# Performance work log

Hardware: AMD Instinct MI355X
Metric: run time of the kernel (lower is better)

The kernel has to match this reference:

```python
import jax, jax.numpy as jnp
import numpy as np

N = 20000
E = 320000
IN_DIM = 128
HID = 64
HEADS = 8
OUT_DIM = 128
NEG_SLOPE = 0.2  # PyG GATConv default leaky_relu slope


def _glorot(key, shape):
    fan_in = shape[0] if len(shape) > 1 else shape[-1]
    return jax.random.normal(key, shape, dtype=jnp.float32) / jnp.sqrt(jnp.float32(fan_in))


def setup_inputs() -> dict:
    key = jax.random.key(0)
    ks = jax.random.split(key, 16)
    x = jax.random.normal(ks[0], (N, IN_DIM), dtype=jnp.float32)
    edge_index = jax.random.randint(ks[1], (2, E), 0, N, dtype=jnp.int32)
    HC = HEADS * HID
    return {
        "x": x,
        "edge_index": edge_index,
        # layer 1: in -> heads*hid (concat)
        "W1": _glorot(ks[2], (IN_DIM, HC)),
        "a_src1": _glorot(ks[3], (HEADS, HID)),
        "a_dst1": _glorot(ks[4], (HEADS, HID)),
        "b1": jnp.zeros((HC,), jnp.float32),
        # layer 2: heads*hid -> heads*hid (concat)
        "W2": _glorot(ks[5], (HC, HC)),
        "a_src2": _glorot(ks[6], (HEADS, HID)),
        "a_dst2": _glorot(ks[7], (HEADS, HID)),
        "b2": jnp.zeros((HC,), jnp.float32),
        # layer 3: heads*hid -> out, heads=1, concat=False
        "W3": _glorot(ks[8], (HC, OUT_DIM)),
        "a_src3": _glorot(ks[9], (1, OUT_DIM)),
        "a_dst3": _glorot(ks[10], (1, OUT_DIM)),
        "b3": jnp.zeros((OUT_DIM,), jnp.float32),
    }


def _gat_layer(x, src, dst, W, a_src, a_dst, b, heads, concat):
    # x: [N, F_in] -> h: [N, H, C]
    n = x.shape[0]
    h = (x @ W).reshape(n, heads, -1)
    # per-node attention half-logits: [N, H]
    al_src = jnp.sum(h * a_src[None], axis=-1)
    al_dst = jnp.sum(h * a_dst[None], axis=-1)
    # per-edge logits with leaky relu: [E, H]
    e = jax.nn.leaky_relu(al_src[src] + al_dst[dst], NEG_SLOPE)
    # segment softmax over incoming edges of each dst node
    emax = jax.ops.segment_max(e, dst, num_segments=n)
    ex = jnp.exp(e - emax[dst])
    den = jax.ops.segment_sum(ex, dst, num_segments=n)
    alpha = ex / (den[dst] + 1e-16)
    # weighted scatter-aggregate of source features: [E, H, C] -> [N, H, C]
    out = jax.ops.segment_sum(h[src] * alpha[:, :, None], dst, num_segments=n)
    out = out.reshape(n, -1) if concat else out.mean(axis=1)
    return out + b


def reference(x, edge_index, W1, a_src1, a_dst1, b1, W2, a_src2, a_dst2, b2,
              W3, a_src3, a_dst3, b3):
    # PyG GATConv adds self-loops by default
    loops = jnp.arange(N, dtype=edge_index.dtype)
    src = jnp.concatenate([edge_index[0], loops])
    dst = jnp.concatenate([edge_index[1], loops])
    # eval mode: dropout is identity
    h = _gat_layer(x, src, dst, W1, a_src1, a_dst1, b1, HEADS, True)
    h = jax.nn.elu(h)
    h = _gat_layer(h, src, dst, W2, a_src2, a_dst2, b2, HEADS, True)
    h = jax.nn.elu(h)
    out = _gat_layer(h, src, dst, W3, a_src3, a_dst3, b3, 1, False)
    return out
```

## Files before the change

kernel.cpp:

```cpp
#include <hip/hip_runtime.h>
#include <math.h>

#define NN 20000
#define EE 320000
#define ETOT 340000
#define NHEADS 8
#define HID 64
#define HCV 512
#define IND 128
#define OUTD 128
#define NEG_SLOPE 0.2f
#define LOG2E 1.4426950408889634f

typedef __attribute__((ext_vector_type(8))) _Float16 half8;
typedef __attribute__((ext_vector_type(4))) _Float16 half4;
typedef __attribute__((ext_vector_type(4))) float floatx4;

#define S1 (IND * HCV)
#define S2 (HCV * HCV)
#define S3 (HCV * OUTD)
#define XTOT (NN * IND)

#define NT1 64
#define NT2 320
#define NT_TOT 384
#define XB 2500
__global__ __launch_bounds__(256) void prep_kernel(const float* __restrict__ W1,
                                                   const float* __restrict__ W2,
                                                   const float* __restrict__ W3,
                                                   const float* __restrict__ x,
                                                   _Float16* __restrict__ T1,
                                                   _Float16* __restrict__ T2,
                                                   _Float16* __restrict__ T3,
                                                   _Float16* __restrict__ xh,
                                                   int* __restrict__ cnt) {
    int b = blockIdx.x;
    int tid = threadIdx.x;
    if (b < NT_TOT) {
        __shared__ _Float16 tile[32][34];
        const float* W; _Float16* T; int K, N, tb;
        if (b < NT1)      { W = W1; T = T1; K = IND; N = HCV;  tb = b; }
        else if (b < NT2) { W = W2; T = T2; K = HCV; N = HCV;  tb = b - NT1; }
        else              { W = W3; T = T3; K = HCV; N = OUTD; tb = b - NT2; }
        int ntn = N >> 5;
        int k0 = (tb / ntn) * 32, n0 = (tb % ntn) * 32;
        int tx = tid & 31, ty0 = tid >> 5;
        #pragma unroll
        for (int i = 0; i < 4; i++) {
            int ty = ty0 + 8 * i;
            tile[ty][tx] = (_Float16)W[(size_t)(k0 + ty) * N + n0 + tx];
        }
        __syncthreads();
        #pragma unroll
        for (int i = 0; i < 4; i++) {
            int ty = ty0 + 8 * i;
            T[(size_t)(n0 + ty) * K + k0 + tx] = tile[tx][ty];
        }
    } else if (b < NT_TOT + XB) {
        int idx = (b - NT_TOT) * 256 + tid;
        int j = idx * 4;
        float4 v = *(const float4*)&x[j];
        half4 o;
        o[0] = (_Float16)v.x; o[1] = (_Float16)v.y;
        o[2] = (_Float16)v.z; o[3] = (_Float16)v.w;
        *(half4*)&xh[j] = o;
    } else {
        int idx = (b - NT_TOT - XB) * 256 + tid;
        if (idx < NN) cnt[idx] = 0;
    }
}


__global__ void count_kernel(const int* __restrict__ ei, int* __restrict__ cnt) {
    int i = blockIdx.x * blockDim.x + threadIdx.x;
    if (i >= ETOT) return;
    int v = (i < EE) ? ei[EE + i] : (i - EE);
    atomicAdd(&cnt[v], 1);
}

#define SCH 20
__global__ __launch_bounds__(1024) void scan_kernel(const int* __restrict__ cnt,
                                                    int* __restrict__ row_ptr,
                                                    int* __restrict__ cursor) {
    __shared__ int wtot[16];
    __shared__ int woff[16];
    int t = threadIdx.x;
    int lane = t & 63;
    int wid = t >> 6;
    int base = t * SCH;
    int vals[SCH];
    int s = 0;
    #pragma unroll
    for (int i = 0; i < SCH; i++) {
        int idx = base + i;
        int v = (idx < NN) ? cnt[idx] : 0;
        vals[i] = v;
        s += v;
    }
    int incl = s;
    #pragma unroll
    for (int off = 1; off < 64; off <<= 1) {
        int u = __shfl_up(incl, off);
        if (lane >= off) incl += u;
    }
    int excl = incl - s;
    if (lane == 63) wtot[wid] = incl;
    __syncthreads();
    if (t == 0) {
        int run = 0;
        #pragma unroll
        for (int j = 0; j < 16; j++) { woff[j] = run; run += wtot[j]; }
        row_ptr[NN] = run;
    }
    __syncthreads();
    int run = woff[wid] + excl;
    #pragma unroll
    for (int i = 0; i < SCH; i++) {
        int idx = base + i;
        if (idx < NN) { row_ptr[idx] = run; cursor[idx] = run; run += vals[i]; }
    }
}

__global__ void fill_kernel(const int* __restrict__ ei, int* __restrict__ cursor,
                            int* __restrict__ csr_src) {
    int i = blockIdx.x * blockDim.x + threadIdx.x;
    if (i >= ETOT) return;
    int u, v;
    if (i < EE) { u = ei[i]; v = ei[EE + i]; }
    else        { u = i - EE; v = i - EE; }
    int pos = atomicAdd(&cursor[v], 1);
    csr_src[pos] = u;
}

#define BK 32
__global__ __launch_bounds__(512) void gemm_al(const _Float16* __restrict__ A,
                                               const _Float16* __restrict__ Bt,
                                               _Float16* __restrict__ C16,
                                               const float* __restrict__ a_src,
                                               const float* __restrict__ a_dst,
                                               float* __restrict__ als2,
                                               float* __restrict__ ald2,
                                               int M, int K) {
    __shared__ _Float16 sA[128 * BK];
    __shared__ _Float16 sB[128 * BK];
    __shared__ float psum_s[4][128];
    __shared__ float psum_d[4][128];
    int tid = threadIdx.x;
    int lane = tid & 63;
    int wid = tid >> 6;
    int wv_m = wid >> 2;
    int wv_n = wid & 3;
    int m0 = blockIdx.x * 128, n0 = blockIdx.y * 128;
    int quad = lane >> 4;
    int l15 = lane & 15;

    int phys = wid * 1024 + lane * 16;
    int logical = phys ^ (((phys >> 7) & 3) << 4);
    int lrow = logical >> 6;
    int lcol = (logical >> 4) & 3;
    int gmA = m0 + lrow;
    const _Float16* gA = A + (size_t)gmA * K + lcol * 8;
    const _Float16* gB = Bt + (size_t)(n0 + lrow) * K + lcol * 8;
    bool aok = (gmA < M);
    _Float16* lA = sA + wid * 512;
    _Float16* lB = sB + wid * 512;

    int ra[4], rb[2];
    #pragma unroll
    for (int i = 0; i < 4; i++) {
        int lb = (wv_m * 64 + i * 16 + l15) * 64 + quad * 16;
        ra[i] = lb ^ (((lb >> 7) & 3) << 4);
    }
    #pragma unroll
    for (int j = 0; j < 2; j++) {
        int lb = (wv_n * 32 + j * 16 + l15) * 64 + quad * 16;
        rb[j] = lb ^ (((lb >> 7) & 3) << 4);
    }

    floatx4 acc[4][2] = {};

    for (int k0 = 0; k0 < K; k0 += BK) {
        if (aok)
            __builtin_amdgcn_global_load_lds(
                (const __attribute__((address_space(1))) void*)(gA + k0),
                (__attribute__((address_space(3))) void*)lA, 16, 0, 0);
        __builtin_amdgcn_global_load_lds(
            (const __attribute__((address_space(1))) void*)(gB + k0),
            (__attribute__((address_space(3))) void*)lB, 16, 0, 0);
        __syncthreads();
        half8 a[4], b[2];
        #pragma unroll
        for (int i = 0; i < 4; i++)
            a[i] = *(const half8*)((const char*)sA + ra[i]);
        #pragma unroll
        for (int j = 0; j < 2; j++)
            b[j] = *(const half8*)((const char*)sB + rb[j]);
        #pragma unroll
        for (int i = 0; i < 4; i++)
            #pragma unroll
            for (int j = 0; j < 2; j++)
                acc[i][j] = __builtin_amdgcn_mfma_f32_16x16x32_f16(a[i], b[j], acc[i][j], 0, 0, 0);
        __syncthreads();
    }
    #pragma unroll
    for (int i = 0; i < 4; i++) {
        #pragma unroll
        for (int r = 0; r < 4; r++) {
            int gm = m0 + wv_m * 64 + i * 16 + quad * 4 + r;
            if (gm < M) {
                #pragma unroll
                for (int j = 0; j < 2; j++)
                    C16[(size_t)gm * HCV + n0 + wv_n * 32 + j * 16 + l15] = (_Float16)acc[i][j][r];
            }
        }
    }
    int h0 = n0 >> 6;
    int hh = h0 + (wv_n >> 1);
    float as_v[2], ad_v[2];
    #pragma unroll
    for (int j = 0; j < 2; j++) {
        int dim = (wv_n * 32 + j * 16 + l15) & 63;
        as_v[j] = a_src[hh * HID + dim] * LOG2E;
        ad_v[j] = a_dst[hh * HID + dim] * LOG2E;
    }
    #pragma unroll
    for (int i = 0; i < 4; i++) {
        #pragma unroll
        for (int r = 0; r < 4; r++) {
            float ps = acc[i][0][r] * as_v[0] + acc[i][1][r] * as_v[1];
            float pd = acc[i][0][r] * ad_v[0] + acc[i][1][r] * ad_v[1];
            #pragma unroll
            for (int off = 1; off <= 8; off <<= 1) {
                ps += __shfl_xor(ps, off);
                pd += __shfl_xor(pd, off);
            }
            if (l15 == 0) {
                int row = wv_m * 64 + i * 16 + quad * 4 + r;
                psum_s[wv_n][row] = ps;
                psum_d[wv_n][row] = pd;
            }
        }
    }
    __syncthreads();
    if (tid < 128) {
        int gm = m0 + tid;
        if (gm < M) {
            als2[(size_t)h0 * NN + gm]       = psum_s[0][tid] + psum_s[1][tid];
            als2[(size_t)(h0 + 1) * NN + gm] = psum_s[2][tid] + psum_s[3][tid];
            ald2[(size_t)h0 * NN + gm]       = psum_d[0][tid] + psum_d[1][tid];
            ald2[(size_t)(h0 + 1) * NN + gm] = psum_d[2][tid] + psum_d[3][tid];
        }
    }
}

#define LDK 40
__global__ __launch_bounds__(256) void gemm3(const _Float16* __restrict__ A,
                                             const _Float16* __restrict__ Bt,
                                             _Float16* __restrict__ C16,
                                             const float* __restrict__ a_src,
                                             const float* __restrict__ a_dst,
                                             float* __restrict__ als,
                                             float* __restrict__ ald,
                                             int M, int K) {
    __shared__ _Float16 sA[64 * LDK];
    __shared__ _Float16 sB[128 * LDK];
    __shared__ float psum_s[4][64];
    __shared__ float psum_d[4][64];
    int tid = threadIdx.x;
    int lane = tid & 63;
    int wv = tid >> 6;
    int m0 = blockIdx.x * 64;
    int quad = lane >> 4;
    int l15 = lane & 15;
    int arow = tid >> 2;
    int ac4 = tid & 3;

    floatx4 acc[4][2] = {};

    for (int k0 = 0; k0 < K; k0 += 32) {
        {
            int gm = m0 + arow;
            int4 va;
            if (gm < M && arow < 64) va = *(const int4*)&A[(size_t)gm * K + k0 + ac4 * 8];
            else                     va = make_int4(0, 0, 0, 0);
            if (arow < 64) *(int4*)&sA[arow * LDK + ac4 * 8] = va;
            #pragma unroll
            for (int r = 0; r < 2; r++) {
                int gn = arow + r * 64;
                int4 vb = *(const int4*)&Bt[(size_t)gn * K + k0 + ac4 * 8];
                *(int4*)&sB[(arow + r * 64) * LDK + ac4 * 8] = vb;
            }
        }
        __syncthreads();
        half8 a[4], b[2];
        #pragma unroll
        for (int i = 0; i < 4; i++)
            a[i] = *(const half8*)&sA[(i * 16 + l15) * LDK + quad * 8];
        #pragma unroll
        for (int j = 0; j < 2; j++)
            b[j] = *(const half8*)&sB[(wv * 32 + j * 16 + l15) * LDK + quad * 8];
        #pragma unroll
        for (int i = 0; i < 4; i++)
            #pragma unroll
            for (int j = 0; j < 2; j++)
                acc[i][j] = __builtin_amdgcn_mfma_f32_16x16x32_f16(a[i], b[j], acc[i][j], 0, 0, 0);
        __syncthreads();
    }
    #pragma unroll
    for (int i = 0; i < 4; i++) {
        #pragma unroll
        for (int r = 0; r < 4; r++) {
            int gm = m0 + i * 16 + quad * 4 + r;
            if (gm < M) {
                #pragma unroll
                for (int j = 0; j < 2; j++)
                    C16[(size_t)gm * OUTD + wv * 32 + j * 16 + l15] = (_Float16)acc[i][j][r];
            }
        }
    }
    float as_v[2], ad_v[2];
    #pragma unroll
    for (int j = 0; j < 2; j++) {
        as_v[j] = a_src[wv * 32 + j * 16 + l15] * LOG2E;
        ad_v[j] = a_dst[wv * 32 + j * 16 + l15] * LOG2E;
    }
    #pragma unroll
    for (int i = 0; i < 4; i++) {
        #pragma unroll
        for (int r = 0; r < 4; r++) {
            float ps = acc[i][0][r] * as_v[0] + acc[i][1][r] * as_v[1];
            float pd = acc[i][0][r] * ad_v[0] + acc[i][1][r] * ad_v[1];
            #pragma unroll
            for (int off = 1; off <= 8; off <<= 1) {
                ps += __shfl_xor(ps, off);
                pd += __shfl_xor(pd, off);
            }
            if (l15 == 0) {
                int row = i * 16 + quad * 4 + r;
                psum_s[wv][row] = ps;
                psum_d[wv][row] = pd;
            }
        }
    }
    __syncthreads();
    if (tid < 64) {
        int gm = m0 + tid;
        if (gm < M) {
            als[gm] = psum_s[0][tid] + psum_s[1][tid] + psum_s[2][tid] + psum_s[3][tid];
            ald[gm] = psum_d[0][tid] + psum_d[1][tid] + psum_d[2][tid] + psum_d[3][tid];
        }
    }
}

__global__ __launch_bounds__(256) void gather_kernel(const _Float16* __restrict__ h,
                                                     const int* __restrict__ row_ptr,
                                                     const int* __restrict__ csr_src,
                                                     const float* __restrict__ als2,
                                                     const float* __restrict__ ald2,
                                                     const float* __restrict__ bias,
                                                     _Float16* __restrict__ gout) {
    int tid = threadIdx.x;
    int lane = tid & 63;
    int wid = tid >> 6;
    int bid = blockIdx.x;
    int hd = bid & 7;
    int dl = lane & 7;
    int es = (lane >> 3) & 1;
    int sub = lane >> 4;
    int v = (bid >> 3) * 16 + wid * 4 + sub;
    if (v >= NN) return;
    const float* asl = als2 + (size_t)hd * NN;
    float adst = ald2[(size_t)hd * NN + v];
    int s0 = row_ptr[v], s1 = row_ptr[v + 1];
    int mid = (s0 + s1 + 1) >> 1;
    int jb = es ? mid : s0;
    int je = es ? s1 : mid;
    const _Float16* hh = h + hd * HID + dl * 8;
    float acc[8] = {};
    float l = 0.f;
    int j = jb;
    for (; j + 4 <= je; j += 4) {
        int u[4]; float p[4]; half8 xv[4];
        #pragma unroll
        for (int e = 0; e < 4; e++) u[e] = csr_src[j + e];
        #pragma unroll
        for (int e = 0; e < 4; e++) xv[e] = *(const half8*)&hh[(size_t)u[e] * HCV];
        #pragma unroll
        for (int e = 0; e < 4; e++) {
            float t = asl[u[e]] + adst;
            t = (t > 0.f) ? t : NEG_SLOPE * t;
            p[e] = exp2f(fminf(t, 115.f));
        }
        #pragma unroll
        for (int e = 0; e < 4; e++) {
            l += p[e];
            #pragma unroll
            for (int k = 0; k < 8; k++)
                acc[k] = fmaf(p[e], (float)xv[e][k], acc[k]);
        }
    }
    for (; j < je; j++) {
        int u0 = csr_src[j];
        half8 x0 = *(const half8*)&hh[(size_t)u0 * HCV];
        float t0 = asl[u0] + adst;
        t0 = (t0 > 0.f) ? t0 : NEG_SLOPE * t0;
        float p0 = exp2f(fminf(t0, 115.f));
        l += p0;
        #pragma unroll
        for (int k = 0; k < 8; k++)
            acc[k] = fmaf(p0, (float)x0[k], acc[k]);
    }
    l += __shfl_xor(l, 8);
    #pragma unroll
    for (int k = 0; k < 8; k++)
        acc[k] += __shfl_xor(acc[k], 8);
    if (es == 0) {
        float inv = 1.f / (l + 1e-16f);
        half8 hv;
        #pragma unroll
        for (int k = 0; k < 8; k++) {
            float o = fmaf(acc[k], inv, bias[hd * HID + dl * 8 + k]);
            o = (o > 0.f) ? o : (__expf(o) - 1.f);
            hv[k] = (_Float16)o;
        }
        half8* dst = (half8*)&gout[(size_t)v * HCV + hd * HID + dl * 8];
        __builtin_nontemporal_store(hv, dst);
    }
}

__global__ __launch_bounds__(256) void gather3_kernel(const _Float16* __restrict__ h,
                                                      const int* __restrict__ row_ptr,
                                                      const int* __restrict__ csr_src,
                                                      const float* __restrict__ als,
                                                      const float* __restrict__ ald,
                                                      const float* __restrict__ bias,
                                                      float* __restrict__ out) {
    int tid = threadIdx.x;
    int lane = tid & 63;
    int wid = tid >> 6;
    int bid = blockIdx.x;
    int dh = bid & 1;
    int dl = lane & 7;
    int es = (lane >> 3) & 1;
    int sub = lane >> 4;
    int l16 = lane & 15;
    int v = (bid >> 1) * 16 + wid * 4 + sub;
    if (v >= NN) return;
    float adst = ald[v];
    int s0 = row_ptr[v], s1 = row_ptr[v + 1];
    float m = -INFINITY;
    for (int j = s0 + l16; j < s1; j += 16) {
        int u = csr_src[j];
        float t = als[u] + adst;
        t = (t > 0.f) ? t : NEG_SLOPE * t;
        m = fmaxf(m, t);
    }
    #pragma unroll
    for (int off = 1; off <= 8; off <<= 1)
        m = fmaxf(m, __shfl_xor(m, off));
    int mid = (s0 + s1 + 1) >> 1;
    int jb = es ? mid : s0;
    int je = es ? s1 : mid;
    const _Float16* hh = h + dh * 64 + dl * 8;
    float acc[8] = {};
    float l = 0.f;
    int j = jb;
    for (; j + 2 <= je; j += 2) {
        int u0 = csr_src[j], u1 = csr_src[j + 1];
        float t0 = als[u0] + adst;
        float t1 = als[u1] + adst;
        t0 = (t0 > 0.f) ? t0 : NEG_SLOPE * t0;
        t1 = (t1 > 0.f) ? t1 : NEG_SLOPE * t1;
        float p0 = exp2f(t0 - m);
        float p1 = exp2f(t1 - m);
        half8 x0 = *(const half8*)&hh[(size_t)u0 * OUTD];
        half8 x1 = *(const half8*)&hh[(size_t)u1 * OUTD];
        l += p0 + p1;
        #pragma unroll
        for (int k = 0; k < 8; k++) {
            acc[k] = fmaf(p0, (float)x0[k], acc[k]);
            acc[k] = fmaf(p1, (float)x1[k], acc[k]);
        }
    }
    if (j < je) {
        int u0 = csr_src[j];
        float t0 = als[u0] + adst;
        t0 = (t0 > 0.f) ? t0 : NEG_SLOPE * t0;
        float p0 = exp2f(t0 - m);
        half8 x0 = *(const half8*)&hh[(size_t)u0 * OUTD];
        l += p0;
        #pragma unroll
        for (int k = 0; k < 8; k++)
            acc[k] = fmaf(p0, (float)x0[k], acc[k]);
    }
    l += __shfl_xor(l, 8);
    #pragma unroll
    for (int k = 0; k < 8; k++)
        acc[k] += __shfl_xor(acc[k], 8);
    if (es == 0) {
        float inv = 1.f / (l + 1e-16f);
        float4 o0, o1;
        o0.x = fmaf(acc[0], inv, bias[dh * 64 + dl * 8 + 0]);
        o0.y = fmaf(acc[1], inv, bias[dh * 64 + dl * 8 + 1]);
        o0.z = fmaf(acc[2], inv, bias[dh * 64 + dl * 8 + 2]);
        o0.w = fmaf(acc[3], inv, bias[dh * 64 + dl * 8 + 3]);
        o1.x = fmaf(acc[4], inv, bias[dh * 64 + dl * 8 + 4]);
        o1.y = fmaf(acc[5], inv, bias[dh * 64 + dl * 8 + 5]);
        o1.z = fmaf(acc[6], inv, bias[dh * 64 + dl * 8 + 6]);
        o1.w = fmaf(acc[7], inv, bias[dh * 64 + dl * 8 + 7]);
        size_t base = (size_t)v * OUTD + dh * 64 + dl * 8;
        *(float4*)&out[base] = o0;
        *(float4*)&out[base + 4] = o1;
    }
}


extern "C" void kernel_launch(void* const* d_in, const int* in_sizes, int n_in,
                              void* d_out, int out_size, void* d_ws, size_t ws_size,
                              hipStream_t stream) {
    const float* x     = (const float*)d_in[0];
    const int*   ei    = (const int*)d_in[1];
    const float* W1    = (const float*)d_in[2];
    const float* as1   = (const float*)d_in[3];
    const float* ad1   = (const float*)d_in[4];
    const float* b1    = (const float*)d_in[5];
    const float* W2    = (const float*)d_in[6];
    const float* as2   = (const float*)d_in[7];
    const float* ad2   = (const float*)d_in[8];
    const float* b2    = (const float*)d_in[9];
    const float* W3    = (const float*)d_in[10];
    const float* as3   = (const float*)d_in[11];
    const float* ad3   = (const float*)d_in[12];
    const float* b3    = (const float*)d_in[13];
    float* out = (float*)d_out;

    size_t off = 0;
    auto carve = [&](size_t bytes) {
        void* p = (char*)d_ws + off;
        off += (bytes + 255) & ~(size_t)255;
        return p;
    };
    int* row_ptr   = (int*)carve((NN + 1) * sizeof(int));
    int* cursor    = (int*)carve(NN * sizeof(int));
    int* csr_src   = (int*)carve(ETOT * sizeof(int));
    _Float16* xh   = (_Float16*)carve((size_t)NN * IND * sizeof(_Float16));
    _Float16* h1   = (_Float16*)carve((size_t)NN * HCV * sizeof(_Float16));
    _Float16* gact = (_Float16*)carve((size_t)NN * HCV * sizeof(_Float16));
    _Float16* hf16 = (_Float16*)carve((size_t)NN * HCV * sizeof(_Float16));
    _Float16* h3   = (_Float16*)carve((size_t)NN * OUTD * sizeof(_Float16));
    float* als     = (float*)carve((size_t)NN * NHEADS * sizeof(float));
    float* ald     = (float*)carve((size_t)NN * NHEADS * sizeof(float));
    _Float16* W1T  = (_Float16*)carve((size_t)S1 * sizeof(_Float16));
    _Float16* W2T  = (_Float16*)carve((size_t)S2 * sizeof(_Float16));
    _Float16* W3T  = (_Float16*)carve((size_t)S3 * sizeof(_Float16));
    _Float16* gact2 = h1;
    (void)ws_size; (void)n_in; (void)in_sizes; (void)out_size;

    dim3 blk(256);

    int prep_blocks = NT_TOT + XB + (NN + 255) / 256;
    prep_kernel<<<prep_blocks, blk, 0, stream>>>(W1, W2, W3, x, W1T, W2T, W3T, xh, cursor);

    count_kernel<<<(ETOT + 255) / 256, blk, 0, stream>>>(ei, cursor);
    scan_kernel<<<1, 1024, 0, stream>>>(cursor, row_ptr, cursor);
    fill_kernel<<<(ETOT + 255) / 256, blk, 0, stream>>>(ei, cursor, csr_src);

    int mt64 = (NN + 63) / 64;
    int mt128 = (NN + 127) / 128;
    int nb4 = (NN + 15) / 16;

    gemm_al<<<dim3(mt128, HCV / 128), dim3(512), 0, stream>>>(xh, W1T, h1, as1, ad1, als, ald, NN, IND);
    gather_kernel<<<dim3(nb4 * 8), blk, 0, stream>>>(h1, row_ptr, csr_src, als, ald, b1, gact);

    gemm_al<<<dim3(mt128, HCV / 128), dim3(512), 0, stream>>>(gact, W2T, hf16, as2, ad2, als, ald, NN, HCV);
    gather_kernel<<<dim3(nb4 * 8), blk, 0, stream>>>(hf16, row_ptr, csr_src, als, ald, b2, gact2);

    gemm3<<<dim3(mt64, 1), blk, 0, stream>>>(gact2, W3T, h3, as3, ad3, als, ald, NN, HCV);
    gather3_kernel<<<dim3(nb4 * 2), blk, 0, stream>>>(h3, row_ptr, csr_src, als, ald, b3, out);
}
```

Before: 309.6 us.

## Rewrite gemm3 with direct global-to-LDS loads, swizzled LDS, 128-row tiles

The layer-3 GEMM now uses 512 threads and 128-row tiles. It loads A and B tiles through global_load_lds straight into XOR-swizzled shared memory, following the scheme already used in gemm_al, instead of staging them through registers into padded LDS. Separately, the leaky-relu select in the gather kernels is replaced by fmaxf(t, slope*t). The GEMM change aims to cut load latency and bank conflicts, but it halves the grid to about 157 blocks, which risks underfilling the GPU.

```diff
diff --git a/kernel.cpp b/kernel.cpp
--- a/kernel.cpp
+++ b/kernel.cpp
@@ -253,8 +253,7 @@
     }
 }
 
-#define LDK 40
-__global__ __launch_bounds__(256) void gemm3(const _Float16* __restrict__ A,
+__global__ __launch_bounds__(512) void gemm3(const _Float16* __restrict__ A,
                                              const _Float16* __restrict__ Bt,
                                              _Float16* __restrict__ C16,
                                              const float* __restrict__ a_src,
@@ -262,43 +261,60 @@
                                              float* __restrict__ als,
                                              float* __restrict__ ald,
                                              int M, int K) {
-    __shared__ _Float16 sA[64 * LDK];
-    __shared__ _Float16 sB[128 * LDK];
-    __shared__ float psum_s[4][64];
-    __shared__ float psum_d[4][64];
+    __shared__ _Float16 sA[128 * BK];
+    __shared__ _Float16 sB[128 * BK];
+    __shared__ float psum_s[4][128];
+    __shared__ float psum_d[4][128];
     int tid = threadIdx.x;
     int lane = tid & 63;
-    int wv = tid >> 6;
-    int m0 = blockIdx.x * 64;
+    int wid = tid >> 6;
+    int wv_m = wid >> 2;
+    int wv_n = wid & 3;
+    int m0 = blockIdx.x * 128;
     int quad = lane >> 4;
     int l15 = lane & 15;
-    int arow = tid >> 2;
-    int ac4 = tid & 3;
+
+    int phys = wid * 1024 + lane * 16;
+    int logical = phys ^ (((phys >> 7) & 3) << 4);
+    int lrow = logical >> 6;
+    int lcol = (logical >> 4) & 3;
+    int gmA = m0 + lrow;
+    const _Float16* gA = A + (size_t)gmA * K + lcol * 8;
+    const _Float16* gB = Bt + (size_t)lrow * K + lcol * 8;
+    bool aok = (gmA < M);
+    _Float16* lA = sA + wid * 512;
+    _Float16* lB = sB + wid * 512;
+
+    int ra[4], rb[2];
+    #pragma unroll
+    for (int i = 0; i < 4; i++) {
+        int lb = (wv_m * 64 + i * 16 + l15) * 64 + quad * 16;
+        ra[i] = lb ^ (((lb >> 7) & 3) << 4);
+    }
+    #pragma unroll
+    for (int j = 0; j < 2; j++) {
+        int lb = (wv_n * 32 + j * 16 + l15) * 64 + quad * 16;
+        rb[j] = lb ^ (((lb >> 7) & 3) << 4);
+    }
 
     floatx4 acc[4][2] = {};
 
-    for (int k0 = 0; k0 < K; k0 += 32) {
-        {
-            int gm = m0 + arow;
-            int4 va;
-            if (gm < M && arow < 64) va = *(const int4*)&A[(size_t)gm * K + k0 + ac4 * 8];
-            else                     va = make_int4(0, 0, 0, 0);
-            if (arow < 64) *(int4*)&sA[arow * LDK + ac4 * 8] = va;
-            #pragma unroll
-            for (int r = 0; r < 2; r++) {
-                int gn = arow + r * 64;
-                int4 vb = *(const int4*)&Bt[(size_t)gn * K + k0 + ac4 * 8];
-                *(int4*)&sB[(arow + r * 64) * LDK + ac4 * 8] = vb;
-            }
-        }
+    for (int k0 = 0; k0 < K; k0 += BK) {
+        if (aok)
+            __builtin_amdgcn_global_load_lds(
+                (const __attribute__((address_space(1))) void*)(gA + k0),
+                (__attribute__((address_space(3))) void*)lA, 16, 0, 0);
+        __builtin_amdgcn_global_load_lds(
+            (const __attribute__((address_space(1))) void*)(gB + k0),
+            (__attribute__((address_space(3))) void*)lB, 16, 0, 0);
         __syncthreads();
         half8 a[4], b[2];
         #pragma unroll
         for (int i = 0; i < 4; i++)
-            a[i] = *(const half8*)&sA[(i * 16 + l15) * LDK + quad * 8];
+            a[i] = *(const half8*)((const char*)sA + ra[i]);
         #pragma unroll
         for (int j = 0; j < 2; j++)
-            b[j] = *(const half8*)&sB[(wv * 32 + j * 16 + l15) * LDK + quad * 8];
+            b[j] = *(const half8*)((const char*)sB + rb[j]);
         #pragma unroll
         for (int i = 0; i < 4; i++)
             #pragma unroll
@@ -310,19 +326,20 @@
     for (int i = 0; i < 4; i++) {
         #pragma unroll
         for (int r = 0; r < 4; r++) {
-            int gm = m0 + i * 16 + quad * 4 + r;
+            int gm = m0 + wv_m * 64 + i * 16 + quad * 4 + r;
             if (gm < M) {
                 #pragma unroll
                 for (int j = 0; j < 2; j++)
-                    C16[(size_t)gm * OUTD + wv * 32 + j * 16 + l15] = (_Float16)acc[i][j][r];
+                    C16[(size_t)gm * OUTD + wv_n * 32 + j * 16 + l15] = (_Float16)acc[i][j][r];
             }
         }
     }
     float as_v[2], ad_v[2];
     #pragma unroll
     for (int j = 0; j < 2; j++) {
-        as_v[j] = a_src[wv * 32 + j * 16 + l15] * LOG2E;
-        ad_v[j] = a_dst[wv * 32 + j * 16 + l15] * LOG2E;
+        int dim = wv_n * 32 + j * 16 + l15;
+        as_v[j] = a_src[dim] * LOG2E;
+        ad_v[j] = a_dst[dim] * LOG2E;
     }
     #pragma unroll
     for (int i = 0; i < 4; i++) {
@@ -336,14 +353,14 @@
                 pd += __shfl_xor(pd, off);
             }
             if (l15 == 0) {
-                int row = i * 16 + quad * 4 + r;
-                psum_s[wv][row] = ps;
-                psum_d[wv][row] = pd;
+                int row = wv_m * 64 + i * 16 + quad * 4 + r;
+                psum_s[wv_n][row] = ps;
+                psum_d[wv_n][row] = pd;
             }
         }
     }
     __syncthreads();
-    if (tid < 64) {
+    if (tid < 128) {
         int gm = m0 + tid;
         if (gm < M) {
             als[gm] = psum_s[0][tid] + psum_s[1][tid] + psum_s[2][tid] + psum_s[3][tid];
@@ -388,7 +405,7 @@
         #pragma unroll
         for (int e = 0; e < 4; e++) {
             float t = asl[u[e]] + adst;
-            t = (t > 0.f) ? t : NEG_SLOPE * t;
+            t = fmaxf(t, NEG_SLOPE * t);
             p[e] = exp2f(fminf(t, 115.f));
         }
         #pragma unroll
@@ -403,7 +420,7 @@
         int u0 = csr_src[j];
         half8 x0 = *(const half8*)&hh[(size_t)u0 * HCV];
         float t0 = asl[u0] + adst;
-        t0 = (t0 > 0.f) ? t0 : NEG_SLOPE * t0;
+        t0 = fmaxf(t0, NEG_SLOPE * t0);
         float p0 = exp2f(fminf(t0, 115.f));
         l += p0;
         #pragma unroll
@@ -452,7 +469,7 @@
     for (int j = s0 + l16; j < s1; j += 16) {
         int u = csr_src[j];
         float t = als[u] + adst;
-        t = (t > 0.f) ? t : NEG_SLOPE * t;
+        t = fmaxf(t, NEG_SLOPE * t);
         m = fmaxf(m, t);
     }
     #pragma unroll
@@ -469,8 +486,8 @@
         int u0 = csr_src[j], u1 = csr_src[j + 1];
         float t0 = als[u0] + adst;
         float t1 = als[u1] + adst;
-        t0 = (t0 > 0.f) ? t0 : NEG_SLOPE * t0;
-        t1 = (t1 > 0.f) ? t1 : NEG_SLOPE * t1;
+        t0 = fmaxf(t0, NEG_SLOPE * t0);
+        t1 = fmaxf(t1, NEG_SLOPE * t1);
         float p0 = exp2f(t0 - m);
         float p1 = exp2f(t1 - m);
         half8 x0 = *(const half8*)&hh[(size_t)u0 * OUTD];
@@ -485,7 +502,7 @@
     if (j < je) {
         int u0 = csr_src[j];
         float t0 = als[u0] + adst;
-        t0 = (t0 > 0.f) ? t0 : NEG_SLOPE * t0;
+        t0 = fmaxf(t0, NEG_SLOPE * t0);
         float p0 = exp2f(t0 - m);
         half8 x0 = *(const half8*)&hh[(size_t)u0 * OUTD];
         l += p0;
@@ -565,7 +582,6 @@
     scan_kernel<<<1, 1024, 0, stream>>>(cursor, row_ptr, cursor);
     fill_kernel<<<(ETOT + 255) / 256, blk, 0, stream>>>(ei, cursor, csr_src);
 
-    int mt64 = (NN + 63) / 64;
     int mt128 = (NN + 127) / 128;
     int nb4 = (NN + 15) / 16;
 
@@ -575,6 +591,6 @@
     gemm_al<<<dim3(mt128, HCV / 128), dim3(512), 0, stream>>>(gact, W2T, hf16, as2, ad2, als, ald, NN, HCV);
     gather_kernel<<<dim3(nb4 * 8), blk, 0, stream>>>(hf16, row_ptr, csr_src, als, ald, b2, gact2);
 
-    gemm3<<<dim3(mt64, 1), blk, 0, stream>>>(gact2, W3T, h3, as3, ad3, als, ald, NN, HCV);
+    gemm3<<<dim3(mt128, 1), dim3(512), 0, stream>>>(gact2, W3T, h3, as3, ad3, als, ald, NN, HCV);
     gather3_kernel<<<dim3(nb4 * 2), blk, 0, stream>>>(h3, row_ptr, csr_src, als, ald, b3, out);
 }
```

Result: no change. 310.8 us (+0.4%).
